# Optimization experiments

Measured on AMD Instinct MI355X. Metric: run time of the kernel, lower is better.

Reference implementation:

```python
import jax, jax.numpy as jnp
import numpy as np

NUM_HEADS = 12


def setup_inputs() -> dict:
    key = jax.random.key(0)
    ks = jax.random.split(key, 5)
    R, C, B, E = 256, 256, 1, 768
    s = 1.0 / np.sqrt(E)
    x = jax.random.normal(ks[0], (R, C, B, E), dtype=jnp.float32)
    Wq = jax.random.normal(ks[1], (E, E), dtype=jnp.float32) * s
    Wk = jax.random.normal(ks[2], (E, E), dtype=jnp.float32) * s
    Wv = jax.random.normal(ks[3], (E, E), dtype=jnp.float32) * s
    Wo = jax.random.normal(ks[4], (E, E), dtype=jnp.float32) * s
    z = jnp.zeros((E,), dtype=jnp.float32)
    return {"x": x, "Wq": Wq, "bq": z, "Wk": Wk, "bk": z,
            "Wv": Wv, "bv": z, "Wo": Wo, "bo": z}


def reference(x, Wq, bq, Wk, bk, Wv, bv, Wo, bo):
    R, C, B, E = x.shape
    H = NUM_HEADS
    Dh = E // H
    # align scaling: head_dim**-0.5 / sqrt(num_rows)
    scaling = (Dh ** -0.5) / jnp.sqrt(jnp.asarray(R, x.dtype))
    q = (x @ Wq.T + bq).reshape(R, C, B, H, Dh) * scaling
    k = (x @ Wk.T + bk).reshape(R, C, B, H, Dh)
    v = (x @ Wv.T + bv).reshape(R, C, B, H, Dh)
    # scores reduce over the row axis r BEFORE the shared softmax: [H,B,C,C]
    attn_weights = jnp.einsum('rinhd,rjnhd->hnij', q, k)
    attn_probs = jax.nn.softmax(attn_weights, axis=-1)  # dropout=0
    # shared probs applied to every row's values
    context = jnp.einsum('hnij,rjnhd->rinhd', attn_probs, v).reshape(R, C, B, E)
    output = context @ Wo.T + bo
    return (output, attn_probs)
```

## Files before the change

### kernel.cpp

```cpp
#include <hip/hip_runtime.h>
#include <cstdint>

typedef _Float16 f16;
typedef _Float16 f16x8 __attribute__((ext_vector_type(8)));
typedef float    f32x4 __attribute__((ext_vector_type(4)));

#define OFF_XH   0UL
#define OFF_QT   100663296UL
#define OFF_KT   201326592UL
#define OFF_VT   301989888UL
#define OFF_WQ   402653184UL
#define OFF_WK   403832832UL
#define OFF_WV   405012480UL
#define OFF_WO   406192128UL
#define OFF_PH   407371776UL

__global__ __launch_bounds__(256) void cast_f32_f16(const float* __restrict__ in,
                                                    f16* __restrict__ out, int n8) {
    int i = blockIdx.x * 256 + threadIdx.x;
    if (i >= n8) return;
    const float4* p = (const float4*)in;
    float4 a = p[2*i], b = p[2*i+1];
    f16x8 o;
    o[0]=(f16)a.x; o[1]=(f16)a.y; o[2]=(f16)a.z; o[3]=(f16)a.w;
    o[4]=(f16)b.x; o[5]=(f16)b.y; o[6]=(f16)b.z; o[7]=(f16)b.w;
    ((f16x8*)out)[i] = o;
}

enum { MODE_QK = 0, MODE_V = 1, MODE_SPLIT = 2, MODE_CTX = 3, MODE_OUT = 4 };

__device__ __forceinline__ void gl_lds16(const f16* g, f16* l) {
    auto gp = (const __attribute__((address_space(1))) f16*)(g);
    auto lp = (__attribute__((address_space(3))) f16*)(l);
    __builtin_amdgcn_global_load_lds(gp, lp, 16, 0, 0);
}

template<int MODE>
__global__ __launch_bounds__(256) void gemm_fast(
    const f16* __restrict__ A, const f16* __restrict__ B,
    float* __restrict__ outF, f16* __restrict__ outH,
    const float* __restrict__ bias, float scale,
    int lda, int ldb, int K)
{
    __shared__ f16 As[128*64];
    __shared__ f16 Bs[128*64];
    const int tid = threadIdx.x;
    const int wv = tid >> 6, ln = tid & 63;
    const int lrow = ln & 15, quad = ln >> 4;
    const int wm = wv >> 1, wn = wv & 1;
    const int m0 = blockIdx.y * 128;
    const int n0 = blockIdx.x * 128;
    const int z = blockIdx.z;
    int h = 0, sp = 0;
    if constexpr (MODE == MODE_SPLIT) {
        h = z >> 4; sp = z & 15;
        A += (long)h*4194304 + sp*1024;
        B += (long)h*4194304 + sp*1024;
    } else if constexpr (MODE == MODE_CTX) {
        A += (long)z * 65536;
        B += (long)z * 4194304;
    }

    const int srow = wv*32 + (ln >> 3);
    const int scol = ((ln & 7) ^ (srow & 7)) << 3;
    const f16* ga = A + (long)(m0 + srow)*lda + scol;
    const f16* gb = B + (long)(n0 + srow)*ldb + scol;

    f32x4 acc[4][4] = {};

    for (int k0 = 0; k0 < K; k0 += 64) {
        __syncthreads();
        #pragma unroll
        for (int t = 0; t < 4; t++) {
            gl_lds16(ga + (long)t*8*lda, As + (wv*4 + t)*512);
            gl_lds16(gb + (long)t*8*ldb, Bs + (wv*4 + t)*512);
        }
        ga += 64; gb += 64;
        __syncthreads();
        #pragma unroll
        for (int ks = 0; ks < 2; ks++) {
            const int slot = ((ks*4 + quad) ^ (lrow & 7)) << 3;
            f16x8 af[4], bf[4];
            #pragma unroll
            for (int i = 0; i < 4; i++)
                af[i] = *(const f16x8*)&As[(wm*64 + i*16 + lrow)*64 + slot];
            #pragma unroll
            for (int j = 0; j < 4; j++)
                bf[j] = *(const f16x8*)&Bs[(wn*64 + j*16 + lrow)*64 + slot];
            #pragma unroll
            for (int i = 0; i < 4; i++)
                #pragma unroll
                for (int j = 0; j < 4; j++)
                    acc[i][j] = __builtin_amdgcn_mfma_f32_16x16x32_f16(af[i], bf[j], acc[i][j], 0, 0, 0);
        }
    }

    #pragma unroll
    for (int i = 0; i < 4; i++) {
        #pragma unroll
        for (int j = 0; j < 4; j++) {
            #pragma unroll
            for (int r = 0; r < 4; r++) {
                int m = m0 + wm*64 + i*16 + quad*4 + r;
                int n = n0 + wn*64 + j*16 + lrow;
                float v = acc[i][j][r];
                if constexpr (MODE == MODE_QK) {
                    v = (v + bias[n]) * scale;
                    outH[(((long)((n>>6)*256 + (m&255))*256 + (m>>8))<<6) + (n&63)] = (f16)v;
                } else if constexpr (MODE == MODE_V) {
                    v = v + bias[n];
                    outH[(((long)((n>>6)*256 + (m>>8))*64 + (n&63))<<8) + (m&255)] = (f16)v;
                } else if constexpr (MODE == MODE_SPLIT) {
                    outF[(long)sp*786432 + h*65536 + m*256 + n] = v;
                } else if constexpr (MODE == MODE_CTX) {
                    outH[((long)((n>>6)*256 + m))*768 + z*64 + (n&63)] = (f16)v;
                } else {
                    outF[(long)m*768 + n] = v + bias[n];
                }
            }
        }
    }
}

__global__ __launch_bounds__(256) void softmax_k(const float* __restrict__ Sp,
                                                 float* __restrict__ pOut,
                                                 f16* __restrict__ Ph) {
    __shared__ float red[8];
    const int row = blockIdx.x;
    const int t = threadIdx.x;
    float v = 0.f;
    #pragma unroll
    for (int s = 0; s < 16; s++)
        v += Sp[(long)s*786432 + (long)row*256 + t];
    float mx = v;
    #pragma unroll
    for (int o = 32; o; o >>= 1) mx = fmaxf(mx, __shfl_xor(mx, o, 64));
    if ((t & 63) == 0) red[t >> 6] = mx;
    __syncthreads();
    mx = fmaxf(fmaxf(red[0], red[1]), fmaxf(red[2], red[3]));
    float e = expf(v - mx);
    float s = e;
    #pragma unroll
    for (int o = 32; o; o >>= 1) s += __shfl_xor(s, o, 64);
    if ((t & 63) == 0) red[4 + (t >> 6)] = s;
    __syncthreads();
    s = red[4] + red[5] + red[6] + red[7];
    float p = e / s;
    pOut[(long)row*256 + t] = p;
    Ph[(long)row*256 + t] = (f16)p;
}

extern "C" void kernel_launch(void* const* d_in, const int* in_sizes, int n_in,
                              void* d_out, int out_size, void* d_ws, size_t ws_size,
                              hipStream_t stream) {
    const float* x  = (const float*)d_in[0];
    const float* Wq = (const float*)d_in[1];
    const float* bq = (const float*)d_in[2];
    const float* Wk = (const float*)d_in[3];
    const float* bk = (const float*)d_in[4];
    const float* Wv = (const float*)d_in[5];
    const float* bv = (const float*)d_in[6];
    const float* Wo = (const float*)d_in[7];
    const float* bo = (const float*)d_in[8];
    float* out   = (float*)d_out;
    float* probs = out + 50331648L;

    char* ws = (char*)d_ws;
    f16*   Xh   = (f16*)(ws + OFF_XH);
    float* Sp   = (float*)(ws + OFF_XH);
    f16*   CTXh = (f16*)(ws + OFF_XH);
    f16*   Qt   = (f16*)(ws + OFF_QT);
    f16*   Kt   = (f16*)(ws + OFF_KT);
    f16*   Vt   = (f16*)(ws + OFF_VT);
    f16*   Wqh  = (f16*)(ws + OFF_WQ);
    f16*   Wkh  = (f16*)(ws + OFF_WK);
    f16*   Wvh  = (f16*)(ws + OFF_WV);
    f16*   Woh  = (f16*)(ws + OFF_WO);
    f16*   Ph   = (f16*)(ws + OFF_PH);

    cast_f32_f16<<<24576, 256, 0, stream>>>(x,  Xh,  6291456);
    cast_f32_f16<<<288,   256, 0, stream>>>(Wq, Wqh, 73728);
    cast_f32_f16<<<288,   256, 0, stream>>>(Wk, Wkh, 73728);
    cast_f32_f16<<<288,   256, 0, stream>>>(Wv, Wvh, 73728);
    cast_f32_f16<<<288,   256, 0, stream>>>(Wo, Woh, 73728);

    dim3 g1(6, 512, 1);
    gemm_fast<MODE_QK><<<g1, 256, 0, stream>>>(Xh, Wqh, nullptr, Qt, bq, 1.0f/128.0f, 768, 768, 768);
    gemm_fast<MODE_QK><<<g1, 256, 0, stream>>>(Xh, Wkh, nullptr, Kt, bk, 1.0f,        768, 768, 768);
    gemm_fast<MODE_V ><<<g1, 256, 0, stream>>>(Xh, Wvh, nullptr, Vt, bv, 1.0f,        768, 768, 768);

    gemm_fast<MODE_SPLIT><<<dim3(2, 2, 192), 256, 0, stream>>>(Qt, Kt, Sp, nullptr, nullptr, 1.0f, 16384, 16384, 1024);

    softmax_k<<<3072, 256, 0, stream>>>(Sp, probs, Ph);

    gemm_fast<MODE_CTX><<<dim3(128, 2, 12), 256, 0, stream>>>(Ph, Vt, nullptr, CTXh, nullptr, 1.0f, 256, 256, 256);

    gemm_fast<MODE_OUT><<<g1, 256, 0, stream>>>(CTXh, Woh, out, nullptr, bo, 1.0f, 768, 768, 768);
}
```

Before: 988.2 us.

## Fuse QKV projections into one GEMM and enlarge tiles to 256x256

```diff
diff --git a/kernel.cpp b/kernel.cpp
--- a/kernel.cpp
+++ b/kernel.cpp
@@ -1,19 +1,17 @@
 #include <hip/hip_runtime.h>
-#include <cstdint>
 
 typedef _Float16 f16;
 typedef _Float16 f16x8 __attribute__((ext_vector_type(8)));
 typedef float    f32x4 __attribute__((ext_vector_type(4)));
 
 #define OFF_XH   0UL
-#define OFF_QT   100663296UL
-#define OFF_KT   201326592UL
+#define OFF_QN   100663296UL
+#define OFF_KN   201326592UL
 #define OFF_VT   301989888UL
-#define OFF_WQ   402653184UL
-#define OFF_WK   403832832UL
-#define OFF_WV   405012480UL
+#define OFF_WQKV 402653184UL
 #define OFF_WO   406192128UL
-#define OFF_PH   407371776UL
+#define OFF_BQKV 407371776UL
+#define OFF_PH   407380992UL
 
 __global__ __launch_bounds__(256) void cast_f32_f16(const float* __restrict__ in,
                                                     f16* __restrict__ out, int n8) {
@@ -27,7 +25,11 @@
     ((f16x8*)out)[i] = o;
 }
 
-enum { MODE_QK = 0, MODE_V = 1, MODE_SPLIT = 2, MODE_CTX = 3, MODE_OUT = 4 };
+__global__ void pack_bias(const float* __restrict__ a, const float* __restrict__ b,
+                          const float* __restrict__ c, float* __restrict__ o) {
+    int t = threadIdx.x;
+    o[t] = a[t]; o[768 + t] = b[t]; o[1536 + t] = c[t];
+}
 
 __device__ __forceinline__ void gl_lds16(const f16* g, f16* l) {
     auto gp = (const __attribute__((address_space(1))) f16*)(g);
@@ -35,62 +37,66 @@
     __builtin_amdgcn_global_load_lds(gp, lp, 16, 0, 0);
 }
 
+enum { MODE_QKV = 0, MODE_SPLIT = 1, MODE_CTX = 2, MODE_OUT = 3 };
+
 template<int MODE>
-__global__ __launch_bounds__(256) void gemm_fast(
+__global__ __launch_bounds__(512) void gemm_big(
     const f16* __restrict__ A, const f16* __restrict__ B,
     float* __restrict__ outF, f16* __restrict__ outH,
-    const float* __restrict__ bias, float scale,
-    int lda, int ldb, int K)
+    const float* __restrict__ bias,
+    int lda, int ldb, int K, long kadv)
 {
-    __shared__ f16 As[128*64];
-    __shared__ f16 Bs[128*64];
+    __shared__ f16 As[256 * 64];
+    __shared__ f16 Bs[256 * 64];
     const int tid = threadIdx.x;
     const int wv = tid >> 6, ln = tid & 63;
     const int lrow = ln & 15, quad = ln >> 4;
     const int wm = wv >> 1, wn = wv & 1;
-    const int m0 = blockIdx.y * 128;
-    const int n0 = blockIdx.x * 128;
+    const int m0 = blockIdx.y * 256;
+    const int n0 = blockIdx.x * 256;
     const int z = blockIdx.z;
-    int h = 0, sp = 0;
+
     if constexpr (MODE == MODE_SPLIT) {
-        h = z >> 4; sp = z & 15;
-        A += (long)h*4194304 + sp*1024;
-        B += (long)h*4194304 + sp*1024;
+        const int h = z >> 4, sp = z & 15;
+        A += (long)h * 64 + (long)sp * 16 * 196608;
+        B += (long)h * 64 + (long)sp * 16 * 196608;
     } else if constexpr (MODE == MODE_CTX) {
         A += (long)z * 65536;
         B += (long)z * 4194304;
     }
 
-    const int srow = wv*32 + (ln >> 3);
-    const int scol = ((ln & 7) ^ (srow & 7)) << 3;
-    const f16* ga = A + (long)(m0 + srow)*lda + scol;
-    const f16* gb = B + (long)(n0 + srow)*ldb + scol;
-
-    f32x4 acc[4][4] = {};
+    const int srow = wv * 8 + (ln >> 3);
+    const int scol = ((ln & 7) ^ (ln >> 3)) << 3;
+    const f16* ga = A + (long)(m0 + srow) * lda + scol;
+    const f16* gb = B + (long)(n0 + srow) * ldb + scol;
+    f16* lA = As + (wv * 64 + ln) * 8;
+    f16* lB = Bs + (wv * 64 + ln) * 8;
+
+    f32x4 acc[4][8] = {};
 
     for (int k0 = 0; k0 < K; k0 += 64) {
         __syncthreads();
         #pragma unroll
-        for (int t = 0; t < 4; t++) {
-            gl_lds16(ga + (long)t*8*lda, As + (wv*4 + t)*512);
-            gl_lds16(gb + (long)t*8*ldb, Bs + (wv*4 + t)*512);
+        for (int q = 0; q < 4; q++) {
+            gl_lds16(ga + (long)q * 64 * lda, lA + q * 4096);
+            gl_lds16(gb + (long)q * 64 * ldb, lB + q * 4096);
         }
-        ga += 64; gb += 64;
+        ga += kadv; gb += kadv;
         __syncthreads();
         #pragma unroll
         for (int ks = 0; ks < 2; ks++) {
-            const int slot = ((ks*4 + quad) ^ (lrow & 7)) << 3;
-            f16x8 af[4], bf[4];
+            const int slot = ((ks * 4 + quad) ^ (lrow & 7)) << 3;
+            f16x8 af[4], bf[8];
             #pragma unroll
             for (int i = 0; i < 4; i++)
-                af[i] = *(const f16x8*)&As[(wm*64 + i*16 + lrow)*64 + slot];
-            #pragma unroll
-            for (int j = 0; j < 4; j++)
-                bf[j] = *(const f16x8*)&Bs[(wn*64 + j*16 + lrow)*64 + slot];
+                af[i] = *(const f16x8*)&As[(wm * 64 + i * 16 + lrow) * 64 + slot];
+            #pragma unroll
+            for (int j = 0; j < 8; j++)
+                bf[j] = *(const f16x8*)&Bs[(wn * 128 + j * 16 + lrow) * 64 + slot];
             #pragma unroll
             for (int i = 0; i < 4; i++)
                 #pragma unroll
-                for (int j = 0; j < 4; j++)
+                for (int j = 0; j < 8; j++)
                     acc[i][j] = __builtin_amdgcn_mfma_f32_16x16x32_f16(af[i], bf[j], acc[i][j], 0, 0, 0);
         }
     }
@@ -98,24 +104,28 @@
     #pragma unroll
     for (int i = 0; i < 4; i++) {
         #pragma unroll
-        for (int j = 0; j < 4; j++) {
+        for (int j = 0; j < 8; j++) {
             #pragma unroll
             for (int r = 0; r < 4; r++) {
-                int m = m0 + wm*64 + i*16 + quad*4 + r;
-                int n = n0 + wn*64 + j*16 + lrow;
+                int m = m0 + wm * 64 + i * 16 + quad * 4 + r;
+                int n = n0 + wn * 128 + j * 16 + lrow;
                 float v = acc[i][j][r];
-                if constexpr (MODE == MODE_QK) {
-                    v = (v + bias[n]) * scale;
-                    outH[(((long)((n>>6)*256 + (m&255))*256 + (m>>8))<<6) + (n&63)] = (f16)v;
-                } else if constexpr (MODE == MODE_V) {
-                    v = v + bias[n];
-                    outH[(((long)((n>>6)*256 + (m>>8))*64 + (n&63))<<8) + (m&255)] = (f16)v;
+                if constexpr (MODE == MODE_QKV) {
+                    v += bias[n];
+                    if (n0 < 768) {
+                        outH[(long)m * 768 + n] = (f16)(v * (1.0f / 128.0f));
+                    } else if (n0 < 1536) {
+                        (outH + 50331648L)[(long)m * 768 + (n - 768)] = (f16)v;
+                    } else {
+                        int np = n - 1536;
+                        (outH + 100663296L)[(((long)((np >> 6) * 256 + (m >> 8)) << 6) + (np & 63)) * 256 + (m & 255)] = (f16)v;
+                    }
                 } else if constexpr (MODE == MODE_SPLIT) {
-                    outF[(long)sp*786432 + h*65536 + m*256 + n] = v;
+                    outF[(long)(z & 15) * 786432 + (long)(z >> 4) * 65536 + m * 256 + n] = v;
                 } else if constexpr (MODE == MODE_CTX) {
-                    outH[((long)((n>>6)*256 + m))*768 + z*64 + (n&63)] = (f16)v;
+                    outH[((long)((n >> 6) * 256 + m)) * 768 + z * 64 + (n & 63)] = (f16)v;
                 } else {
-                    outF[(long)m*768 + n] = v + bias[n];
+                    outF[(long)m * 768 + n] = v + bias[n];
                 }
             }
         }
@@ -131,7 +141,7 @@
     float v = 0.f;
     #pragma unroll
     for (int s = 0; s < 16; s++)
-        v += Sp[(long)s*786432 + (long)row*256 + t];
+        v += Sp[(long)s * 786432 + (long)row * 256 + t];
     float mx = v;
     #pragma unroll
     for (int o = 32; o; o >>= 1) mx = fmaxf(mx, __shfl_xor(mx, o, 64));
@@ -146,8 +156,8 @@
     __syncthreads();
     s = red[4] + red[5] + red[6] + red[7];
     float p = e / s;
-    pOut[(long)row*256 + t] = p;
-    Ph[(long)row*256 + t] = (f16)p;
+    pOut[(long)row * 256 + t] = p;
+    Ph[(long)row * 256 + t] = (f16)p;
 }
 
 extern "C" void kernel_launch(void* const* d_in, const int* in_sizes, int n_in,
@@ -169,31 +179,32 @@
     f16*   Xh   = (f16*)(ws + OFF_XH);
     float* Sp   = (float*)(ws + OFF_XH);
     f16*   CTXh = (f16*)(ws + OFF_XH);
-    f16*   Qt   = (f16*)(ws + OFF_QT);
-    f16*   Kt   = (f16*)(ws + OFF_KT);
-    f16*   Vt   = (f16*)(ws + OFF_VT);
-    f16*   Wqh  = (f16*)(ws + OFF_WQ);
-    f16*   Wkh  = (f16*)(ws + OFF_WK);
-    f16*   Wvh  = (f16*)(ws + OFF_WV);
+    f16*   Qn   = (f16*)(ws + OFF_QN);
+    f16*   Kn   = (f16*)(ws + OFF_KN);
+    f16*   Vt2  = (f16*)(ws + OFF_VT);
+    f16*   Wqkv = (f16*)(ws + OFF_WQKV);
     f16*   Woh  = (f16*)(ws + OFF_WO);
+    float* bqkv = (float*)(ws + OFF_BQKV);
     f16*   Ph   = (f16*)(ws + OFF_PH);
 
-    cast_f32_f16<<<24576, 256, 0, stream>>>(x,  Xh,  6291456);
-    cast_f32_f16<<<288,   256, 0, stream>>>(Wq, Wqh, 73728);
-    cast_f32_f16<<<288,   256, 0, stream>>>(Wk, Wkh, 73728);
-    cast_f32_f16<<<288,   256, 0, stream>>>(Wv, Wvh, 73728);
-    cast_f32_f16<<<288,   256, 0, stream>>>(Wo, Woh, 73728);
-
-    dim3 g1(6, 512, 1);
-    gemm_fast<MODE_QK><<<g1, 256, 0, stream>>>(Xh, Wqh, nullptr, Qt, bq, 1.0f/128.0f, 768, 768, 768);
-    gemm_fast<MODE_QK><<<g1, 256, 0, stream>>>(Xh, Wkh, nullptr, Kt, bk, 1.0f,        768, 768, 768);
-    gemm_fast<MODE_V ><<<g1, 256, 0, stream>>>(Xh, Wvh, nullptr, Vt, bv, 1.0f,        768, 768, 768);
-
-    gemm_fast<MODE_SPLIT><<<dim3(2, 2, 192), 256, 0, stream>>>(Qt, Kt, Sp, nullptr, nullptr, 1.0f, 16384, 16384, 1024);
+    cast_f32_f16<<<24576, 256, 0, stream>>>(x,  Xh, 6291456);
+    cast_f32_f16<<<288, 256, 0, stream>>>(Wq, Wqkv,           73728);
+    cast_f32_f16<<<288, 256, 0, stream>>>(Wk, Wqkv +  589824, 73728);
+    cast_f32_f16<<<288, 256, 0, stream>>>(Wv, Wqkv + 1179648, 73728);
+    cast_f32_f16<<<288, 256, 0, stream>>>(Wo, Woh,            73728);
+    pack_bias<<<1, 768, 0, stream>>>(bq, bk, bv, bqkv);
+
+    gemm_big<MODE_QKV><<<dim3(9, 256), 512, 0, stream>>>(
+        Xh, Wqkv, nullptr, Qn, bqkv, 768, 768, 768, 64);
+
+    gemm_big<MODE_SPLIT><<<dim3(1, 1, 192), 512, 0, stream>>>(
+        Qn, Kn, Sp, nullptr, nullptr, 768, 768, 1024, 196608);
 
     softmax_k<<<3072, 256, 0, stream>>>(Sp, probs, Ph);
 
-    gemm_fast<MODE_CTX><<<dim3(128, 2, 12), 256, 0, stream>>>(Ph, Vt, nullptr, CTXh, nullptr, 1.0f, 256, 256, 256);
-
-    gemm_fast<MODE_OUT><<<g1, 256, 0, stream>>>(CTXh, Woh, out, nullptr, bo, 1.0f, 768, 768, 768);
-}
+    gemm_big<MODE_CTX><<<dim3(64, 1, 12), 512, 0, stream>>>(
+        Ph, Vt2, nullptr, CTXh, nullptr, 256, 256, 256, 64);
+
+    gemm_big<MODE_OUT><<<dim3(3, 256), 512, 0, stream>>>(
+        CTXh, Woh, out, nullptr, bo, 768, 768, 768, 64);
+}
```

New measurement: 1.085 ms. 9.8% more time.
